# Kernel optimization log

Measured on AMD Instinct MI355X. Metric: run time of the kernel, lower is better.

The kernel has to match this reference:

```python
import jax, jax.numpy as jnp
import numpy as np

SQ, B, NP, HN = 2048, 2, 16, 64  # [seq, batch, heads, head_dim]

def setup_inputs() -> dict:
    key = jax.random.key(0)
    kq, kk, kv = jax.random.split(key, 3)
    return {
        "query": jax.random.normal(kq, (SQ, B, NP, HN), dtype=jnp.float32),
        "key":   jax.random.normal(kk, (SQ, B, NP, HN), dtype=jnp.float32),
        "value": jax.random.normal(kv, (SQ, B, NP, HN), dtype=jnp.float32),
    }

def reference(query, key, value):
    sq, b, nheads, hn = query.shape
    # NOTE: original module computes norm_factor=sqrt(hn) but never applies it;
    # scores are UNscaled QK^T, replicated faithfully here.
    scores = jnp.einsum('sbnh,tbnh->bnst', query, key)          # [b, np, sq, sk]
    probs = jax.nn.softmax(scores, axis=-1)                      # mask=None -> plain softmax
    # dropout is deterministic (train=False default) -> identity
    context = jnp.einsum('bnst,tbnh->sbnh', probs, value)        # [sq, b, np, hn]
    return context.reshape(sq, b, nheads * hn).astype(jnp.float32)
```

## Files before the change

### kernel.cpp

```cpp
#include <hip/hip_runtime.h>
#include <math.h>
#include <stdint.h>

#define SQ 2048
#define NBH 32
#define HN 64
#define BQ 128
#define BK 64
#define NT (SQ/BK)
#define TOK 2048
#define HSTRIDE (SQ*HN)

typedef _Float16 half2v __attribute__((ext_vector_type(2)));
typedef _Float16 half4v __attribute__((ext_vector_type(4)));
typedef _Float16 half8v __attribute__((ext_vector_type(8)));
typedef float f32x16 __attribute__((ext_vector_type(16)));

__device__ __forceinline__ void async16(const void* g, void* l) {
  __builtin_amdgcn_global_load_lds(
      (const __attribute__((address_space(1))) void*)g,
      (__attribute__((address_space(3))) void*)l, 16, 0, 0);
}

__global__ __launch_bounds__(256) void prep_k(const float* __restrict__ K,
                                              _Float16* __restrict__ Kh) {
  const int t = threadIdx.x;
  const int head = blockIdx.y;
  const int key = blockIdx.x * 64 + (t >> 2);
  const int c0 = (t & 3) * 2;
  const float* src = K + (size_t)key * TOK + head * HN + c0 * 8;
  float4 a = *(const float4*)src;
  float4 b = *(const float4*)(src + 4);
  float4 c = *(const float4*)(src + 8);
  float4 d = *(const float4*)(src + 12);
  half8v h0, h1;
  h0[0]=(_Float16)a.x; h0[1]=(_Float16)a.y; h0[2]=(_Float16)a.z; h0[3]=(_Float16)a.w;
  h0[4]=(_Float16)b.x; h0[5]=(_Float16)b.y; h0[6]=(_Float16)b.z; h0[7]=(_Float16)b.w;
  h1[0]=(_Float16)c.x; h1[1]=(_Float16)c.y; h1[2]=(_Float16)c.z; h1[3]=(_Float16)c.w;
  h1[4]=(_Float16)d.x; h1[5]=(_Float16)d.y; h1[6]=(_Float16)d.z; h1[7]=(_Float16)d.w;
  _Float16* row = Kh + (size_t)head * HSTRIDE + (size_t)key * 64;
  *(half8v*)&row[((c0    ) ^ (key & 7)) * 8] = h0;
  *(half8v*)&row[((c0 + 1) ^ (key & 7)) * 8] = h1;
}

__global__ __launch_bounds__(256) void prep_v(const float* __restrict__ V,
                                              _Float16* __restrict__ Vt) {
  __shared__ _Float16 vs[HN * 64];
  const int t = threadIdx.x;
  const int head = blockIdx.y;
  const int kt = blockIdx.x * 64;
  const int kl = (t >> 3) * 2;
  const int db = (t & 7) * 8;
  const float* src = V + (size_t)(kt + kl) * TOK + head * HN + db;
  float4 a0 = *(const float4*)src;
  float4 a1 = *(const float4*)(src + 4);
  float4 b0 = *(const float4*)(src + TOK);
  float4 b1 = *(const float4*)(src + TOK + 4);
  const float av[8] = {a0.x,a0.y,a0.z,a0.w,a1.x,a1.y,a1.z,a1.w};
  const float bv[8] = {b0.x,b0.y,b0.z,b0.w,b1.x,b1.y,b1.z,b1.w};
  const int u = kl >> 2;
  #pragma unroll
  for (int j = 0; j < 8; ++j) {
    const int dim = db + j;
    const int pos = u ^ (dim & 15);
    half2v h; h[0] = (_Float16)av[j]; h[1] = (_Float16)bv[j];
    *(half2v*)&vs[dim * 64 + pos * 4 + (kl & 3)] = h;
  }
  __syncthreads();
  const int dim = t >> 2;
  const int q = (t & 3) ^ (dim & 3);
  const _Float16* srow = &vs[dim * 64 + q * 16];
  _Float16* drow = Vt + (size_t)head * HSTRIDE + (size_t)dim * SQ + kt + q * 16;
  *(half8v*)&drow[0] = *(const half8v*)&srow[0];
  *(half8v*)&drow[8] = *(const half8v*)&srow[8];
}

__global__ __launch_bounds__(256, 2)
void fattn_mfma(const float* __restrict__ Q, const _Float16* __restrict__ Kh,
                const _Float16* __restrict__ Vt, float* __restrict__ O) {
  __shared__ __align__(16) _Float16 kbf[2][BK * 64];
  __shared__ __align__(16) _Float16 vtf[2][HN * 64];

  const int t = threadIdx.x;
  const int lane = t & 63;
  const int w = t >> 6;
  const int h2 = lane >> 5;
  const int l31 = lane & 31;
  const int q0 = blockIdx.x * BQ + w * 32;
  const int head = blockIdx.y;
  const _Float16* Kp = Kh + (size_t)head * HSTRIDE;
  const _Float16* Vp = Vt + (size_t)head * HSTRIDE;

  half8v qf[4];
  {
    const float* qp = Q + (size_t)(q0 + l31) * TOK + head * HN + 8 * h2;
    #pragma unroll
    for (int ks = 0; ks < 4; ++ks) {
      float4 a = *(const float4*)(qp + 16 * ks);
      float4 b = *(const float4*)(qp + 16 * ks + 4);
      half8v f;
      f[0] = (_Float16)a.x; f[1] = (_Float16)a.y; f[2] = (_Float16)a.z; f[3] = (_Float16)a.w;
      f[4] = (_Float16)b.x; f[5] = (_Float16)b.y; f[6] = (_Float16)b.z; f[7] = (_Float16)b.w;
      qf[ks] = f;
    }
  }

  f32x16 acc0, acc1;
  #pragma unroll
  for (int r = 0; r < 16; ++r) { acc0[r] = 0.f; acc1[r] = 0.f; }
  float m_i = -INFINITY, l_i = 0.f;

  auto stage = [&](int it) {
    const int kt = it * BK;
    const int buf = it & 1;
    #pragma unroll
    for (int i = 0; i < 2; ++i) {
      const int off = w * 1024 + i * 512;
      async16(Kp + (size_t)kt * 64 + off + lane * 8, &kbf[buf][off]);
    }
    #pragma unroll
    for (int i = 0; i < 2; ++i) {
      const int off = w * 1024 + i * 512;
      const int eo = off + lane * 8;
      const int dim = eo >> 6, inner = eo & 63;
      async16(Vp + (size_t)dim * SQ + kt + inner, &vtf[buf][off]);
    }
  };

  stage(0);
  for (int it = 0; it < NT; ++it) {
    __syncthreads();
    if (it + 1 < NT) stage(it + 1);
    const int cur = it & 1;

    f32x16 sf0, sf1;
    {
      f32x16 c0, c1;
      #pragma unroll
      for (int r = 0; r < 16; ++r) { c0[r] = 0.f; c1[r] = 0.f; }
      #pragma unroll
      for (int ks = 0; ks < 4; ++ks) {
        const int pos = ((h2 + 2 * ks) ^ (l31 & 7)) * 8;
        half8v a0v = *(const half8v*)&kbf[cur][l31 * 64 + pos];
        half8v a1v = *(const half8v*)&kbf[cur][(l31 + 32) * 64 + pos];
        c0 = __builtin_amdgcn_mfma_f32_32x32x16_f16(a0v, qf[ks], c0, 0, 0, 0);
        c1 = __builtin_amdgcn_mfma_f32_32x32x16_f16(a1v, qf[ks], c1, 0, 0, 0);
      }
      sf0 = c0; sf1 = c1;
    }

    float mx = -INFINITY;
    #pragma unroll
    for (int r = 0; r < 16; ++r) mx = fmaxf(mx, fmaxf(sf0[r], sf1[r]));
    mx = fmaxf(mx, __shfl_xor(mx, 32, 64));
    const float mnew = fmaxf(m_i, mx);
    const float alpha = __expf(m_i - mnew);
    float rsum = 0.f;
    #pragma unroll
    for (int r = 0; r < 16; ++r) {
      float p0 = __expf(sf0[r] - mnew);
      float p1 = __expf(sf1[r] - mnew);
      sf0[r] = p0; sf1[r] = p1;
      rsum += p0 + p1;
    }
    rsum += __shfl_xor(rsum, 32, 64);
    l_i = l_i * alpha + rsum;
    m_i = mnew;
    #pragma unroll
    for (int r = 0; r < 16; ++r) { acc0[r] *= alpha; acc1[r] *= alpha; }

    #pragma unroll
    for (int ks = 0; ks < 4; ++ks) {
      const int rb = 8 * (ks & 1);
      const f32x16& s = (ks < 2) ? sf0 : sf1;
      union { half8v v8; half2v v2[4]; } pu;
      #pragma unroll
      for (int tt = 0; tt < 4; ++tt) {
        auto pk = __builtin_amdgcn_cvt_pkrtz(s[rb + 2 * tt], s[rb + 2 * tt + 1]);
        pu.v2[tt] = *(half2v*)&pk;
      }
      #pragma unroll
      for (int mbd = 0; mbd < 2; ++mbd) {
        const int dim = l31 + 32 * mbd;
        const int sw = dim & 15;
        union { half8v v8; half4v v4[2]; } au;
        au.v4[0] = *(const half4v*)&vtf[cur][dim * 64 + ((4 * ks + h2)     ^ sw) * 4];
        au.v4[1] = *(const half4v*)&vtf[cur][dim * 64 + ((4 * ks + 2 + h2) ^ sw) * 4];
        if (mbd == 0)
          acc0 = __builtin_amdgcn_mfma_f32_32x32x16_f16(au.v8, pu.v8, acc0, 0, 0, 0);
        else
          acc1 = __builtin_amdgcn_mfma_f32_32x32x16_f16(au.v8, pu.v8, acc1, 0, 0, 0);
      }
    }
  }

  const float invl = 1.f / l_i;
  float* orow = O + (size_t)(q0 + l31) * TOK + head * HN;
  #pragma unroll
  for (int r = 0; r < 16; ++r) {
    const int d = (r & 3) + 8 * (r >> 2) + 4 * h2;
    orow[d]      = acc0[r] * invl;
    orow[d + 32] = acc1[r] * invl;
  }
}

extern "C" void kernel_launch(void* const* d_in, const int* in_sizes, int n_in,
                              void* d_out, int out_size, void* d_ws, size_t ws_size,
                              hipStream_t stream) {
  const float* Q = (const float*)d_in[0];
  const float* K = (const float*)d_in[1];
  const float* V = (const float*)d_in[2];
  float* O = (float*)d_out;
  _Float16* Kh = (_Float16*)d_ws;
  _Float16* Vh = Kh + (size_t)NBH * HSTRIDE;
  prep_k<<<dim3(SQ / 64, NBH), 256, 0, stream>>>(K, Kh);
  prep_v<<<dim3(SQ / 64, NBH), 256, 0, stream>>>(V, Vh);
  fattn_mfma<<<dim3(SQ / BQ, NBH), 256, 0, stream>>>(Q, Kh, Vh, O);
}
```

Measured before the change: 159.7 us.

## Split KV sequence across blocks with merge kernel, fuse K/V prep, use exp2

Splits the key dimension of flash attention into two halves, each handled by its own block (grid z dimension). Each block writes unnormalised partial outputs in fp16 plus per-row max and sum, and a new merge kernel combines the halves. The change also fuses the K and V conversion kernels into one launch, folds log2(e) into Q so the softmax can use exp2, and raises the launch-bounds occupancy hint from 2 to 4. It aims to double the number of blocks (512 instead of 256) to fill the GPU better, at the cost of an extra kernel launch, partial-result traffic, and fp16 rounding of the partial outputs.

```diff
diff --git a/kernel.cpp b/kernel.cpp
--- a/kernel.cpp
+++ b/kernel.cpp
@@ -1,13 +1,14 @@
 #include <hip/hip_runtime.h>
 #include <math.h>
-#include <stdint.h>
 
 #define SQ 2048
 #define NBH 32
 #define HN 64
 #define BQ 128
 #define BK 64
-#define NT (SQ/BK)
+#define NSPLIT 2
+#define KSPLIT (SQ/NSPLIT)
+#define NPH (KSPLIT/BK)
 #define TOK 2048
 #define HSTRIDE (SQ*HN)
 
@@ -21,63 +22,71 @@
       (const __attribute__((address_space(1))) void*)g,
       (__attribute__((address_space(3))) void*)l, 16, 0, 0);
 }
-
-__global__ __launch_bounds__(256) void prep_k(const float* __restrict__ K,
-                                              _Float16* __restrict__ Kh) {
-  const int t = threadIdx.x;
-  const int head = blockIdx.y;
-  const int key = blockIdx.x * 64 + (t >> 2);
-  const int c0 = (t & 3) * 2;
-  const float* src = K + (size_t)key * TOK + head * HN + c0 * 8;
-  float4 a = *(const float4*)src;
-  float4 b = *(const float4*)(src + 4);
-  float4 c = *(const float4*)(src + 8);
-  float4 d = *(const float4*)(src + 12);
-  half8v h0, h1;
-  h0[0]=(_Float16)a.x; h0[1]=(_Float16)a.y; h0[2]=(_Float16)a.z; h0[3]=(_Float16)a.w;
-  h0[4]=(_Float16)b.x; h0[5]=(_Float16)b.y; h0[6]=(_Float16)b.z; h0[7]=(_Float16)b.w;
-  h1[0]=(_Float16)c.x; h1[1]=(_Float16)c.y; h1[2]=(_Float16)c.z; h1[3]=(_Float16)c.w;
-  h1[4]=(_Float16)d.x; h1[5]=(_Float16)d.y; h1[6]=(_Float16)d.z; h1[7]=(_Float16)d.w;
-  _Float16* row = Kh + (size_t)head * HSTRIDE + (size_t)key * 64;
-  *(half8v*)&row[((c0    ) ^ (key & 7)) * 8] = h0;
-  *(half8v*)&row[((c0 + 1) ^ (key & 7)) * 8] = h1;
-}
-
-__global__ __launch_bounds__(256) void prep_v(const float* __restrict__ V,
-                                              _Float16* __restrict__ Vt) {
+__device__ __forceinline__ float fexp2(float x) {
+#if __has_builtin(__builtin_amdgcn_exp2f)
+  return __builtin_amdgcn_exp2f(x);
+#else
+  return exp2f(x);
+#endif
+}
+
+__global__ __launch_bounds__(256) void prep_kv(const float* __restrict__ K,
+                                               const float* __restrict__ V,
+                                               _Float16* __restrict__ Kh,
+                                               _Float16* __restrict__ Vt) {
   __shared__ _Float16 vs[HN * 64];
   const int t = threadIdx.x;
   const int head = blockIdx.y;
-  const int kt = blockIdx.x * 64;
-  const int kl = (t >> 3) * 2;
-  const int db = (t & 7) * 8;
-  const float* src = V + (size_t)(kt + kl) * TOK + head * HN + db;
-  float4 a0 = *(const float4*)src;
-  float4 a1 = *(const float4*)(src + 4);
-  float4 b0 = *(const float4*)(src + TOK);
-  float4 b1 = *(const float4*)(src + TOK + 4);
-  const float av[8] = {a0.x,a0.y,a0.z,a0.w,a1.x,a1.y,a1.z,a1.w};
-  const float bv[8] = {b0.x,b0.y,b0.z,b0.w,b1.x,b1.y,b1.z,b1.w};
-  const int u = kl >> 2;
-  #pragma unroll
-  for (int j = 0; j < 8; ++j) {
-    const int dim = db + j;
-    const int pos = u ^ (dim & 15);
-    half2v h; h[0] = (_Float16)av[j]; h[1] = (_Float16)bv[j];
-    *(half2v*)&vs[dim * 64 + pos * 4 + (kl & 3)] = h;
-  }
-  __syncthreads();
-  const int dim = t >> 2;
-  const int q = (t & 3) ^ (dim & 3);
-  const _Float16* srow = &vs[dim * 64 + q * 16];
-  _Float16* drow = Vt + (size_t)head * HSTRIDE + (size_t)dim * SQ + kt + q * 16;
-  *(half8v*)&drow[0] = *(const half8v*)&srow[0];
-  *(half8v*)&drow[8] = *(const half8v*)&srow[8];
-}
-
-__global__ __launch_bounds__(256, 2)
+  {
+    const int key = blockIdx.x * 64 + (t >> 2);
+    const int c0 = (t & 3) * 2;
+    const float* src = K + (size_t)key * TOK + head * HN + c0 * 8;
+    float4 a = *(const float4*)src;
+    float4 b = *(const float4*)(src + 4);
+    float4 c = *(const float4*)(src + 8);
+    float4 d = *(const float4*)(src + 12);
+    half8v h0, h1;
+    h0[0]=(_Float16)a.x; h0[1]=(_Float16)a.y; h0[2]=(_Float16)a.z; h0[3]=(_Float16)a.w;
+    h0[4]=(_Float16)b.x; h0[5]=(_Float16)b.y; h0[6]=(_Float16)b.z; h0[7]=(_Float16)b.w;
+    h1[0]=(_Float16)c.x; h1[1]=(_Float16)c.y; h1[2]=(_Float16)c.z; h1[3]=(_Float16)c.w;
+    h1[4]=(_Float16)d.x; h1[5]=(_Float16)d.y; h1[6]=(_Float16)d.z; h1[7]=(_Float16)d.w;
+    _Float16* row = Kh + (size_t)head * HSTRIDE + (size_t)key * 64;
+    *(half8v*)&row[((c0    ) ^ (key & 7)) * 8] = h0;
+    *(half8v*)&row[((c0 + 1) ^ (key & 7)) * 8] = h1;
+  }
+  {
+    const int kt = blockIdx.x * 64;
+    const int kl = (t >> 3) * 2;
+    const int db = (t & 7) * 8;
+    const float* src = V + (size_t)(kt + kl) * TOK + head * HN + db;
+    float4 a0 = *(const float4*)src;
+    float4 a1 = *(const float4*)(src + 4);
+    float4 b0 = *(const float4*)(src + TOK);
+    float4 b1 = *(const float4*)(src + TOK + 4);
+    const float av[8] = {a0.x,a0.y,a0.z,a0.w,a1.x,a1.y,a1.z,a1.w};
+    const float bv[8] = {b0.x,b0.y,b0.z,b0.w,b1.x,b1.y,b1.z,b1.w};
+    const int u = kl >> 2;
+    #pragma unroll
+    for (int j = 0; j < 8; ++j) {
+      const int dim = db + j;
+      const int pos = u ^ (dim & 15);
+      half2v h; h[0] = (_Float16)av[j]; h[1] = (_Float16)bv[j];
+      *(half2v*)&vs[dim * 64 + pos * 4 + (kl & 3)] = h;
+    }
+    __syncthreads();
+    const int dim = t >> 2;
+    const int q = (t & 3) ^ (dim & 3);
+    const _Float16* srow = &vs[dim * 64 + q * 16];
+    _Float16* drow = Vt + (size_t)head * HSTRIDE + (size_t)dim * SQ + kt + q * 16;
+    *(half8v*)&drow[0] = *(const half8v*)&srow[0];
+    *(half8v*)&drow[8] = *(const half8v*)&srow[8];
+  }
+}
+
+__global__ __launch_bounds__(256, 4)
 void fattn_mfma(const float* __restrict__ Q, const _Float16* __restrict__ Kh,
-                const _Float16* __restrict__ Vt, float* __restrict__ O) {
+                const _Float16* __restrict__ Vt, _Float16* __restrict__ Op,
+                float2* __restrict__ ML) {
   __shared__ __align__(16) _Float16 kbf[2][BK * 64];
   __shared__ __align__(16) _Float16 vtf[2][HN * 64];
 
@@ -86,21 +95,24 @@
   const int w = t >> 6;
   const int h2 = lane >> 5;
   const int l31 = lane & 31;
-  const int q0 = blockIdx.x * BQ + w * 32;
+  const int qb = blockIdx.x * BQ + w * 32;
   const int head = blockIdx.y;
+  const int sp = blockIdx.z;
+  const int koff = sp * KSPLIT;
   const _Float16* Kp = Kh + (size_t)head * HSTRIDE;
   const _Float16* Vp = Vt + (size_t)head * HSTRIDE;
 
   half8v qf[4];
   {
-    const float* qp = Q + (size_t)(q0 + l31) * TOK + head * HN + 8 * h2;
+    const float* qp = Q + (size_t)(qb + l31) * TOK + head * HN + 8 * h2;
+    const float s = 1.44269504088896f;
     #pragma unroll
     for (int ks = 0; ks < 4; ++ks) {
       float4 a = *(const float4*)(qp + 16 * ks);
       float4 b = *(const float4*)(qp + 16 * ks + 4);
       half8v f;
-      f[0] = (_Float16)a.x; f[1] = (_Float16)a.y; f[2] = (_Float16)a.z; f[3] = (_Float16)a.w;
-      f[4] = (_Float16)b.x; f[5] = (_Float16)b.y; f[6] = (_Float16)b.z; f[7] = (_Float16)b.w;
+      f[0]=(_Float16)(s*a.x); f[1]=(_Float16)(s*a.y); f[2]=(_Float16)(s*a.z); f[3]=(_Float16)(s*a.w);
+      f[4]=(_Float16)(s*b.x); f[5]=(_Float16)(s*b.y); f[6]=(_Float16)(s*b.z); f[7]=(_Float16)(s*b.w);
       qf[ks] = f;
     }
   }
@@ -110,9 +122,9 @@
   for (int r = 0; r < 16; ++r) { acc0[r] = 0.f; acc1[r] = 0.f; }
   float m_i = -INFINITY, l_i = 0.f;
 
-  auto stage = [&](int it) {
-    const int kt = it * BK;
-    const int buf = it & 1;
+  auto stage = [&](int p) {
+    const int kt = koff + p * BK;
+    const int buf = p & 1;
     #pragma unroll
     for (int i = 0; i < 2; ++i) {
       const int off = w * 1024 + i * 512;
@@ -128,10 +140,10 @@
   };
 
   stage(0);
-  for (int it = 0; it < NT; ++it) {
+  for (int p = 0; p < NPH; ++p) {
     __syncthreads();
-    if (it + 1 < NT) stage(it + 1);
-    const int cur = it & 1;
+    if (p + 1 < NPH) stage(p + 1);
+    const int cur = p & 1;
 
     f32x16 sf0, sf1;
     {
@@ -154,12 +166,12 @@
     for (int r = 0; r < 16; ++r) mx = fmaxf(mx, fmaxf(sf0[r], sf1[r]));
     mx = fmaxf(mx, __shfl_xor(mx, 32, 64));
     const float mnew = fmaxf(m_i, mx);
-    const float alpha = __expf(m_i - mnew);
+    const float alpha = fexp2(m_i - mnew);
     float rsum = 0.f;
     #pragma unroll
     for (int r = 0; r < 16; ++r) {
-      float p0 = __expf(sf0[r] - mnew);
-      float p1 = __expf(sf1[r] - mnew);
+      float p0 = fexp2(sf0[r] - mnew);
+      float p1 = fexp2(sf1[r] - mnew);
       sf0[r] = p0; sf1[r] = p1;
       rsum += p0 + p1;
     }
@@ -194,14 +206,49 @@
     }
   }
 
-  const float invl = 1.f / l_i;
-  float* orow = O + (size_t)(q0 + l31) * TOK + head * HN;
+  _Float16* prow = Op + (((size_t)(sp * NBH + head)) * SQ + qb + l31) * HN;
   #pragma unroll
-  for (int r = 0; r < 16; ++r) {
-    const int d = (r & 3) + 8 * (r >> 2) + 4 * h2;
-    orow[d]      = acc0[r] * invl;
-    orow[d + 32] = acc1[r] * invl;
-  }
+  for (int rq = 0; rq < 4; ++rq) {
+    half4v h0, h1;
+    #pragma unroll
+    for (int j = 0; j < 4; ++j) {
+      h0[j] = (_Float16)acc0[4 * rq + j];
+      h1[j] = (_Float16)acc1[4 * rq + j];
+    }
+    *(half4v*)&prow[8 * rq + 4 * h2]      = h0;
+    *(half4v*)&prow[32 + 8 * rq + 4 * h2] = h1;
+  }
+  if (h2 == 0) {
+    float2 ml; ml.x = m_i; ml.y = l_i;
+    ML[((size_t)(sp * NBH + head)) * SQ + qb + l31] = ml;
+  }
+}
+
+__global__ __launch_bounds__(256)
+void merge2(const _Float16* __restrict__ Op, const float2* __restrict__ ML,
+            float* __restrict__ O) {
+  const int gid = blockIdx.x * 256 + threadIdx.x;
+  const int f = gid * 4;
+  const int q = f >> 11;
+  const int rem = f & 2047;
+  const int head = rem >> 6;
+  const int d = rem & 63;
+  const size_t i0 = (size_t)head * SQ + q;
+  const size_t i1 = (size_t)(NBH + head) * SQ + q;
+  const float2 ml0 = ML[i0];
+  const float2 ml1 = ML[i1];
+  const float m = fmaxf(ml0.x, ml1.x);
+  const float w0 = fexp2(ml0.x - m);
+  const float w1 = fexp2(ml1.x - m);
+  const float inv = 1.f / (ml0.y * w0 + ml1.y * w1);
+  half4v a0 = *(const half4v*)(Op + i0 * HN + d);
+  half4v a1 = *(const half4v*)(Op + i1 * HN + d);
+  float4 o;
+  o.x = ((float)a0[0] * w0 + (float)a1[0] * w1) * inv;
+  o.y = ((float)a0[1] * w0 + (float)a1[1] * w1) * inv;
+  o.z = ((float)a0[2] * w0 + (float)a1[2] * w1) * inv;
+  o.w = ((float)a0[3] * w0 + (float)a1[3] * w1) * inv;
+  *(float4*)(O + f) = o;
 }
 
 extern "C" void kernel_launch(void* const* d_in, const int* in_sizes, int n_in,
@@ -213,7 +260,9 @@
   float* O = (float*)d_out;
   _Float16* Kh = (_Float16*)d_ws;
   _Float16* Vh = Kh + (size_t)NBH * HSTRIDE;
-  prep_k<<<dim3(SQ / 64, NBH), 256, 0, stream>>>(K, Kh);
-  prep_v<<<dim3(SQ / 64, NBH), 256, 0, stream>>>(V, Vh);
-  fattn_mfma<<<dim3(SQ / BQ, NBH), 256, 0, stream>>>(Q, Kh, Vh, O);
-}
+  _Float16* Op = Vh + (size_t)NBH * HSTRIDE;
+  float2*   ML = (float2*)(Op + (size_t)NSPLIT * NBH * SQ * HN);
+  prep_kv<<<dim3(SQ / 64, NBH), 256, 0, stream>>>(K, V, Kh, Vh);
+  fattn_mfma<<<dim3(SQ / BQ, NBH, NSPLIT), 256, 0, stream>>>(Q, Kh, Vh, Op, ML);
+  merge2<<<dim3(SQ * NBH * HN / 4 / 256), 256, 0, stream>>>(Op, ML, O);
+}
```

New measurement: 153.2 us. 1.04x faster.
